# Kernel tuning notes

Measured on AMD Instinct MI355X. Metric: run time of the kernel, lower is better.

Reference implementation:

```python
import jax, jax.numpy as jnp
import numpy as np

N_NODES = 100000
N_EDGES = 1000000
IN_DIM = 64
OUT_DIM = 64
EDGE_DIM = 16
LN_EPS = 1e-5
GINE_EPS = 0.0  # PyG GINEConv default eps


def setup_inputs() -> dict:
    key = jax.random.key(0)
    ks = jax.random.split(key, 10)
    s = lambda d: 1.0 / np.sqrt(d)
    x = jax.random.normal(ks[0], (N_NODES, IN_DIM), dtype=jnp.float32)
    edge_index = jax.random.randint(ks[1], (2, N_EDGES), 0, N_NODES, dtype=jnp.int64)
    edge_attr = jax.random.normal(ks[2], (N_EDGES, EDGE_DIM), dtype=jnp.float32)
    # GINEConv internal edge projection Linear(edge_dim, in_dim)
    We = jax.random.uniform(ks[3], (EDGE_DIM, IN_DIM), jnp.float32, -s(EDGE_DIM), s(EDGE_DIM))
    be = jax.random.uniform(ks[4], (IN_DIM,), jnp.float32, -s(EDGE_DIM), s(EDGE_DIM))
    # MLP: Linear(in_dim, out_dim) -> ReLU -> Linear(out_dim, out_dim)
    W1 = jax.random.uniform(ks[5], (IN_DIM, OUT_DIM), jnp.float32, -s(IN_DIM), s(IN_DIM))
    b1 = jax.random.uniform(ks[6], (OUT_DIM,), jnp.float32, -s(IN_DIM), s(IN_DIM))
    W2 = jax.random.uniform(ks[7], (OUT_DIM, OUT_DIM), jnp.float32, -s(OUT_DIM), s(OUT_DIM))
    b2 = jax.random.uniform(ks[8], (OUT_DIM,), jnp.float32, -s(OUT_DIM), s(OUT_DIM))
    ln_gamma = jnp.ones((OUT_DIM,), jnp.float32)
    ln_beta = jnp.zeros((OUT_DIM,), jnp.float32)
    return {"x": x, "edge_index": edge_index, "edge_attr": edge_attr,
            "We": We, "be": be, "W1": W1, "b1": b1, "W2": W2, "b2": b2,
            "ln_gamma": ln_gamma, "ln_beta": ln_beta}


def reference(x, edge_index, edge_attr, We, be, W1, b1, W2, b2, ln_gamma, ln_beta):
    src, dst = edge_index[0], edge_index[1]
    # message: ReLU(x_j + lin(edge_attr))  [E, IN_DIM]
    msg = jax.nn.relu(x[src] + edge_attr @ We + be)
    # scatter-sum into target nodes  [N, IN_DIM]
    aggr = jax.ops.segment_sum(msg, dst, num_segments=x.shape[0])
    h = (1.0 + GINE_EPS) * x + aggr
    # MLP
    h = jax.nn.relu(h @ W1 + b1) @ W2 + b2
    # LayerNorm over last dim
    mu = jnp.mean(h, axis=-1, keepdims=True)
    var = jnp.var(h, axis=-1, keepdims=True)
    h = (h - mu) * jax.lax.rsqrt(var + LN_EPS) * ln_gamma + ln_beta
    return jax.nn.relu(h)
```

## Files before the change

### kernel.cpp

```cpp
#include <hip/hip_runtime.h>

typedef short short8 __attribute__((ext_vector_type(8)));
typedef float f32x4 __attribute__((ext_vector_type(4)));

__device__ __forceinline__ float bf2f(unsigned short b) {
    union { unsigned u; float f; } c;
    c.u = ((unsigned)b) << 16;
    return c.f;
}

__device__ __forceinline__ unsigned short f2bf(float x) {
    union { float f; unsigned u; } c;
    c.f = x;
    unsigned u = c.u;
    u += 0x7fffu + ((u >> 16) & 1u);
    return (unsigned short)(u >> 16);
}

__device__ __forceinline__ float loadf(const void* p, long long i, unsigned isbf) {
    if (isbf) return bf2f(((const unsigned short*)p)[i]);
    return ((const float*)p)[i];
}

__device__ __forceinline__ f32x4 mfma16(short8 a, short8 b, f32x4 c) {
    return __builtin_amdgcn_mfma_f32_16x16x32_bf16(a, b, c, 0, 0, 0);
}

__device__ __forceinline__ float dotbf(uint4 ea, uint4 eb, const float* Wcol) {
    unsigned wds[8] = {ea.x, ea.y, ea.z, ea.w, eb.x, eb.y, eb.z, eb.w};
    float acc = 0.f;
    #pragma unroll
    for (int q = 0; q < 8; ++q) {
        union { unsigned u; float f; } clo, chi;
        clo.u = wds[q] << 16;
        chi.u = wds[q] & 0xffff0000u;
        acc += clo.f * Wcol[2 * q] + chi.f * Wcol[2 * q + 1];
    }
    return acc;
}

__device__ __forceinline__ float dotf32(const float* eap, const float* Wcol) {
    f32x4 e0 = ((const f32x4*)eap)[0];
    f32x4 e1 = ((const f32x4*)eap)[1];
    f32x4 e2 = ((const f32x4*)eap)[2];
    f32x4 e3 = ((const f32x4*)eap)[3];
    float ea[16] = {e0[0], e0[1], e0[2], e0[3],
                    e1[0], e1[1], e1[2], e1[3],
                    e2[0], e2[1], e2[2], e2[3],
                    e3[0], e3[1], e3[2], e3[3]};
    float acc = 0.f;
    #pragma unroll
    for (int k = 0; k < 16; ++k) acc += ea[k] * Wcol[k];
    return acc;
}

__global__ void gine_flag_kernel(const unsigned* gm_bits, const unsigned* ei_bits,
                                 unsigned* flags) {
    if (blockIdx.x == 0 && threadIdx.x == 0) {
        flags[0] = (gm_bits[0] == 0x3F803F80u) ? 1u : 0u;
        unsigned o = 0;
        for (int k = 0; k < 8; ++k) o |= ei_bits[2 * k + 1];
        flags[1] = (o == 0u) ? 1u : 0u;
    }
}

__global__ void gine_zero_kernel(float* p, int n) {
    int t = blockIdx.x * blockDim.x + threadIdx.x;
    if (t < n) p[t] = 0.0f;
}

__global__ void gine_prep_kernel(const void* W1, const void* b1,
                                 const void* W2, const void* b2,
                                 const void* gm, const void* bt,
                                 const void* We, const void* be,
                                 const unsigned* flags,
                                 unsigned short* W1B, unsigned short* W2B,
                                 float* vecs) {
    int t = blockIdx.x * blockDim.x + threadIdx.x;
    unsigned isbf = flags[0];
    if (t < 8192) {
        int which = t >> 12;
        int u = t & 4095;
        int j = u & 7, L = (u >> 3) & 63, ktnt = u >> 9;
        int kt = ktnt >> 2, nt = ktnt & 3;
        int k = kt * 32 + (L >> 4) * 8 + j;
        int c = nt * 16 + (L & 15);
        const void* W = which ? W2 : W1;
        unsigned short v = f2bf(loadf(W, k * 64 + c, isbf));
        if (which) W2B[u] = v; else W1B[u] = v;
    } else if (t < 8448) {
        int u = t - 8192;
        const void* s = (u < 64) ? b1 : (u < 128) ? b2 : (u < 192) ? gm : bt;
        vecs[u] = loadf(s, u & 63, isbf);
    } else if (t < 8512) {
        vecs[256 + (t - 8448)] = loadf(be, t - 8448, isbf);
    } else if (t < 9536) {
        int u = t - 8512;
        vecs[320 + u] = loadf(We, u, isbf);
    }
}

__global__ void gine_hist_kernel(const void* edge_index, const unsigned* flags,
                                 int* count, int E, int N) {
    int t = blockIdx.x * blockDim.x + threadIdx.x;
    int stride = gridDim.x * blockDim.x;
    unsigned is64 = flags[1];
    for (int e = t; e < E; e += stride) {
        long long dst = is64 ? ((const long long*)edge_index)[E + e]
                             : (long long)((const int*)edge_index)[E + e];
        if (dst >= 0 && dst < N) atomicAdd(&count[(int)dst], 1);
    }
}

__global__ void gine_scan1_kernel(const int* count, int* row_start, int* bsum,
                                  int N) {
    __shared__ int s[256];
    int t = threadIdx.x;
    int i = blockIdx.x * 256 + t;
    int v = (i < N) ? count[i] : 0;
    s[t] = v;
    __syncthreads();
    for (int off = 1; off < 256; off <<= 1) {
        int u = (t >= off) ? s[t - off] : 0;
        __syncthreads();
        s[t] += u;
        __syncthreads();
    }
    if (i < N) row_start[i] = s[t] - v;
    if (t == 255) bsum[blockIdx.x] = s[255];
}

__global__ void gine_scan2_kernel(int* bsum, int* bscan, int* row_start,
                                  int nb, int N) {
    __shared__ int s[512];
    int t = threadIdx.x;
    int v = (t < nb) ? bsum[t] : 0;
    s[t] = v;
    __syncthreads();
    for (int off = 1; off < 512; off <<= 1) {
        int u = (t >= off) ? s[t - off] : 0;
        __syncthreads();
        s[t] += u;
        __syncthreads();
    }
    if (t < nb) bscan[t] = s[t] - v;
    if (t == nb - 1) row_start[N] = s[t];
}

__global__ void gine_scan3_kernel(int* row_start, int* cursor,
                                  const int* bscan, int N) {
    int i = blockIdx.x * 256 + threadIdx.x;
    if (i < N) {
        int r = row_start[i] + bscan[blockIdx.x];
        row_start[i] = r;
        cursor[i] = r;
    }
}

__global__ void gine_scatter_kernel(const void* edge_index, const unsigned* flags,
                                    int* cursor, unsigned long long* sorted,
                                    int E, int N) {
    int t = blockIdx.x * blockDim.x + threadIdx.x;
    int stride = gridDim.x * blockDim.x;
    unsigned is64 = flags[1];
    for (int e = t; e < E; e += stride) {
        long long src, dst;
        if (is64) {
            src = ((const long long*)edge_index)[e];
            dst = ((const long long*)edge_index)[E + e];
        } else {
            src = ((const int*)edge_index)[e];
            dst = ((const int*)edge_index)[E + e];
        }
        if (dst < 0 || dst >= N) continue;
        if (src < 0) src = 0;
        if (src >= N) src = N - 1;
        int pos = atomicAdd(&cursor[(int)dst], 1);
        sorted[pos] = ((unsigned long long)(unsigned)e << 32) | (unsigned long long)(unsigned)src;
    }
}

__global__ void gine_scatter2_kernel(const void* edge_index, const void* edge_attr,
                                     const unsigned* flags,
                                     int* cursor, unsigned long long* sorted,
                                     unsigned short* ea_perm, int E, int N) {
    int t = blockIdx.x * blockDim.x + threadIdx.x;
    int stride = gridDim.x * blockDim.x;
    unsigned is64 = flags[1];
    unsigned isbf = flags[0];
    for (int e = t; e < E; e += stride) {
        long long src, dst;
        if (is64) {
            src = ((const long long*)edge_index)[e];
            dst = ((const long long*)edge_index)[E + e];
        } else {
            src = ((const int*)edge_index)[e];
            dst = ((const int*)edge_index)[E + e];
        }
        if (dst < 0 || dst >= N) continue;
        if (src < 0) src = 0;
        if (src >= N) src = N - 1;
        int pos = atomicAdd(&cursor[(int)dst], 1);
        sorted[pos] = ((unsigned long long)(unsigned)e << 32) | (unsigned long long)(unsigned)src;
        if (isbf) {
            const uint4* er = (const uint4*)((const unsigned short*)edge_attr
                                             + (size_t)e * 16);
            uint4 r0 = er[0];
            uint4 r1 = er[1];
            uint4* wp = (uint4*)(ea_perm + (size_t)pos * 16);
            wp[0] = r0;
            wp[1] = r1;
        }
    }
}

__global__ __launch_bounds__(256) void gine_gather2_kernel(
        const void* x, const void* edge_attr,
        const unsigned long long* sorted, const unsigned short* ea_perm,
        const int* row_start, const float* vecs,
        const unsigned* flags, float* h, int N) {
    int w = threadIdx.x >> 6;
    int lane = threadIdx.x & 63;
    int gw = blockIdx.x * 4 + w;
    int nwaves = gridDim.x * 4;
    unsigned isbf = flags[0];

    float Wcol[16];
    #pragma unroll
    for (int k = 0; k < 16; ++k) Wcol[k] = vecs[320 + k * 64 + lane];
    float bev = vecs[256 + lane];

    if (isbf) {
        const unsigned short* xb = (const unsigned short*)x;
        for (int v = gw; v < N; v += nwaves) {
            int beg = row_start[v];
            int end = row_start[v + 1];
            float a0 = bf2f(xb[(size_t)v * 64 + lane]);
            float a1 = 0.f;
            int i = beg;
            for (; i + 2 <= end; i += 2) {
                unsigned long long c0 = sorted[i];
                unsigned long long c1 = sorted[i + 1];
                int src0 = (int)(c0 & 0xffffffffULL);
                int src1 = (int)(c1 & 0xffffffffULL);

                const uint4* p = (const uint4*)(ea_perm + (size_t)i * 16);
                uint4 e00 = p[0], e01 = p[1];
                uint4 e10 = p[2], e11 = p[3];

                float xv0 = bf2f(xb[(size_t)src0 * 64 + lane]);
                float xv1 = bf2f(xb[(size_t)src1 * 64 + lane]);

                float m0 = dotbf(e00, e01, Wcol);
                float m1 = dotbf(e10, e11, Wcol);
                m0 += bev + xv0; if (m0 < 0.f) m0 = 0.f; a0 += m0;
                m1 += bev + xv1; if (m1 < 0.f) m1 = 0.f; a1 += m1;
            }
            for (; i < end; ++i) {
                unsigned long long c = sorted[i];
                int src = (int)(c & 0xffffffffULL);
                const uint4* p = (const uint4*)(ea_perm + (size_t)i * 16);
                uint4 e0 = p[0], e1 = p[1];
                float xv = bf2f(xb[(size_t)src * 64 + lane]);
                float m = dotbf(e0, e1, Wcol);
                m += bev + xv;
                if (m < 0.f) m = 0.f;
                a0 += m;
            }
            h[(long long)v * 64 + lane] = a0 + a1;
        }
    } else {
        const float* xf  = (const float*)x;
        const float* eaf = (const float*)edge_attr;
        for (int v = gw; v < N; v += nwaves) {
            int beg = row_start[v];
            int end = row_start[v + 1];
            float a0 = xf[(size_t)v * 64 + lane];
            float a1 = 0.f;
            int i = beg;
            for (; i + 2 <= end; i += 2) {
                unsigned long long c0 = sorted[i];
                unsigned long long c1 = sorted[i + 1];
                int src0 = (int)(c0 & 0xffffffffULL), eid0 = (int)(c0 >> 32);
                int src1 = (int)(c1 & 0xffffffffULL), eid1 = (int)(c1 >> 32);
                float xv0 = xf[(size_t)src0 * 64 + lane];
                float xv1 = xf[(size_t)src1 * 64 + lane];
                float m0 = dotf32(eaf + (size_t)eid0 * 16, Wcol);
                float m1 = dotf32(eaf + (size_t)eid1 * 16, Wcol);
                m0 += bev + xv0; if (m0 < 0.f) m0 = 0.f; a0 += m0;
                m1 += bev + xv1; if (m1 < 0.f) m1 = 0.f; a1 += m1;
            }
            for (; i < end; ++i) {
                unsigned long long c = sorted[i];
                int src = (int)(c & 0xffffffffULL);
                int eid = (int)(c >> 32);
                float xv = xf[(size_t)src * 64 + lane];
                float m = dotf32(eaf + (size_t)eid * 16, Wcol);
                m += bev + xv;
                if (m < 0.f) m = 0.f;
                a0 += m;
            }
            h[(long long)v * 64 + lane] = a0 + a1;
        }
    }
}

__global__ __launch_bounds__(256, 4) void gine_gather_kernel(
        const void* x, const void* edge_attr,
        const unsigned long long* sorted,
        const int* row_start, const float* vecs,
        const unsigned* flags, float* h, int N) {
    int w = threadIdx.x >> 6;
    int lane = threadIdx.x & 63;
    int gw = blockIdx.x * 4 + w;
    int nwaves = gridDim.x * 4;
    unsigned isbf = flags[0];

    float Wcol[16];
    #pragma unroll
    for (int k = 0; k < 16; ++k) Wcol[k] = vecs[320 + k * 64 + lane];
    float bev = vecs[256 + lane];

    if (isbf) {
        const unsigned short* xb  = (const unsigned short*)x;
        const unsigned short* eab = (const unsigned short*)edge_attr;
        for (int v = gw; v < N; v += nwaves) {
            int beg = row_start[v];
            int end = row_start[v + 1];
            float a0 = bf2f(xb[(size_t)v * 64 + lane]);
            float a1 = 0.f, a2 = 0.f, a3 = 0.f;
            int i = beg;
            for (; i + 4 <= end; i += 4) {
                unsigned long long c0 = sorted[i];
                unsigned long long c1 = sorted[i + 1];
                unsigned long long c2 = sorted[i + 2];
                unsigned long long c3 = sorted[i + 3];
                int src0 = (int)(c0 & 0xffffffffULL), eid0 = (int)(c0 >> 32);
                int src1 = (int)(c1 & 0xffffffffULL), eid1 = (int)(c1 >> 32);
                int src2 = (int)(c2 & 0xffffffffULL), eid2 = (int)(c2 >> 32);
                int src3 = (int)(c3 & 0xffffffffULL), eid3 = (int)(c3 >> 32);

                float xv0 = bf2f(xb[(size_t)src0 * 64 + lane]);
                float xv1 = bf2f(xb[(size_t)src1 * 64 + lane]);
                float xv2 = bf2f(xb[(size_t)src2 * 64 + lane]);
                float xv3 = bf2f(xb[(size_t)src3 * 64 + lane]);

                const uint4* p0 = (const uint4*)(eab + (size_t)eid0 * 16);
                const uint4* p1 = (const uint4*)(eab + (size_t)eid1 * 16);
                const uint4* p2 = (const uint4*)(eab + (size_t)eid2 * 16);
                const uint4* p3 = (const uint4*)(eab + (size_t)eid3 * 16);
                uint4 e00 = p0[0], e01 = p0[1];
                uint4 e10 = p1[0], e11 = p1[1];
                uint4 e20 = p2[0], e21 = p2[1];
                uint4 e30 = p3[0], e31 = p3[1];

                float m0 = dotbf(e00, e01, Wcol);
                float m1 = dotbf(e10, e11, Wcol);
                float m2 = dotbf(e20, e21, Wcol);
                float m3 = dotbf(e30, e31, Wcol);
                m0 += bev + xv0; if (m0 < 0.f) m0 = 0.f; a0 += m0;
                m1 += bev + xv1; if (m1 < 0.f) m1 = 0.f; a1 += m1;
                m2 += bev + xv2; if (m2 < 0.f) m2 = 0.f; a2 += m2;
                m3 += bev + xv3; if (m3 < 0.f) m3 = 0.f; a3 += m3;
            }
            for (; i < end; ++i) {
                unsigned long long c = sorted[i];
                int src = (int)(c & 0xffffffffULL);
                int eid = (int)(c >> 32);
                float xv = bf2f(xb[(size_t)src * 64 + lane]);
                const uint4* p0 = (const uint4*)(eab + (size_t)eid * 16);
                uint4 e0 = p0[0], e1 = p0[1];
                float m = dotbf(e0, e1, Wcol);
                m += bev + xv;
                if (m < 0.f) m = 0.f;
                a0 += m;
            }
            h[(long long)v * 64 + lane] = (a0 + a1) + (a2 + a3);
        }
    } else {
        const float* xf  = (const float*)x;
        const float* eaf = (const float*)edge_attr;
        for (int v = gw; v < N; v += nwaves) {
            int beg = row_start[v];
            int end = row_start[v + 1];
            float a0 = xf[(size_t)v * 64 + lane];
            float a1 = 0.f;
            int i = beg;
            for (; i + 2 <= end; i += 2) {
                unsigned long long c0 = sorted[i];
                unsigned long long c1 = sorted[i + 1];
                int src0 = (int)(c0 & 0xffffffffULL), eid0 = (int)(c0 >> 32);
                int src1 = (int)(c1 & 0xffffffffULL), eid1 = (int)(c1 >> 32);
                float xv0 = xf[(size_t)src0 * 64 + lane];
                float xv1 = xf[(size_t)src1 * 64 + lane];
                float m0 = dotf32(eaf + (size_t)eid0 * 16, Wcol);
                float m1 = dotf32(eaf + (size_t)eid1 * 16, Wcol);
                m0 += bev + xv0; if (m0 < 0.f) m0 = 0.f; a0 += m0;
                m1 += bev + xv1; if (m1 < 0.f) m1 = 0.f; a1 += m1;
            }
            for (; i < end; ++i) {
                unsigned long long c = sorted[i];
                int src = (int)(c & 0xffffffffULL);
                int eid = (int)(c >> 32);
                float xv = xf[(size_t)src * 64 + lane];
                float m = dotf32(eaf + (size_t)eid * 16, Wcol);
                m += bev + xv;
                if (m < 0.f) m = 0.f;
                a0 += m;
            }
            h[(long long)v * 64 + lane] = a0 + a1;
        }
    }
}

__global__ void GINEBlock_49795850830259_kernel(
    const void* x, const void* edge_index, const void* edge_attr,
    const void* We, const void* be, const unsigned* flags,
    float* aggr, int E, int N, int n0, int n1) {
    int wid  = (blockIdx.x * blockDim.x + threadIdx.x) >> 6;
    int lane = threadIdx.x & 63;
    if (wid >= E) return;

    unsigned isbf = flags[0];
    unsigned is64 = flags[1];

    long long src, dst;
    if (is64) {
        src = ((const long long*)edge_index)[wid];
        dst = ((const long long*)edge_index)[E + wid];
    } else {
        src = ((const int*)edge_index)[wid];
        dst = ((const int*)edge_index)[E + wid];
    }
    if (src < 0 || src >= N || dst < n0 || dst >= n1) return;

    float eav = 0.0f;
    if (lane < 16) eav = loadf(edge_attr, (long long)wid * 16 + lane, isbf);

    float acc = loadf(be, lane, isbf);
    for (int k = 0; k < 16; ++k)
        acc += __shfl(eav, k, 64) * loadf(We, k * 64 + lane, isbf);

    acc += loadf(x, src * 64 + lane, isbf);
    if (acc < 0.0f) acc = 0.0f;

    atomicAdd(aggr + (dst - n0) * 64 + lane, acc);
}

__global__ void gine_addx_kernel(const void* x, float* aggr,
                                 const unsigned* flags, int n0, int n1) {
    int t = blockIdx.x * blockDim.x + threadIdx.x;
    int total = (n1 - n0) * 64;
    if (t >= total) return;
    unsigned isbf = flags[0];
    aggr[t] += loadf(x, (long long)n0 * 64 + t, isbf);
}

__global__ __launch_bounds__(256) void gine_node_mfma_kernel(
    const float* h, const unsigned short* W1B, const unsigned short* W2B,
    const float* vecs, const unsigned* flags, void* out, int n0, int n1) {
    __shared__ float Tlds[4][16 * 68];
    int w = threadIdx.x >> 6;
    int L = threadIdx.x & 63;
    int g = L >> 4, m = L & 15;
    int nb = n0 + (blockIdx.x * 4 + w) * 16;
    if (nb >= n1) return;
    unsigned isbf = flags[0];

    const float* b1f = vecs;
    const float* b2f = vecs + 64;
    const float* gmf = vecs + 128;
    const float* btf = vecs + 192;

    int node = nb + m;
    if (node >= n1) node = n1 - 1;
    long long rel = node - n0;

    short8 ahi[2], alo[2];
    for (int kt = 0; kt < 2; ++kt) {
        int fb = kt * 32 + g * 8;
        const float* hp = h + rel * 64 + fb;
        f32x4 a0 = *(const f32x4*)hp;
        f32x4 a1 = *(const f32x4*)(hp + 4);
        for (int j = 0; j < 8; ++j) {
            float hv = (j < 4) ? a0[j] : a1[j - 4];
            unsigned short hb = f2bf(hv);
            float lo = hv - bf2f(hb);
            ahi[kt][j] = (short)hb;
            alo[kt][j] = (short)f2bf(lo);
        }
    }

    float t16[16];
    for (int nt = 0; nt < 4; ++nt) {
        short8 bp0 = *(const short8*)(W1B + ((size_t)(0 * 4 + nt) * 64 + L) * 8);
        short8 bp1 = *(const short8*)(W1B + ((size_t)(1 * 4 + nt) * 64 + L) * 8);
        f32x4 acc = {0.f, 0.f, 0.f, 0.f};
        acc = mfma16(ahi[0], bp0, acc);
        acc = mfma16(ahi[1], bp1, acc);
        acc = mfma16(alo[0], bp0, acc);
        acc = mfma16(alo[1], bp1, acc);
        float bias = b1f[nt * 16 + m];
        for (int r = 0; r < 4; ++r) {
            float v = acc[r] + bias;
            t16[nt * 4 + r] = v > 0.f ? v : 0.f;
        }
    }

    float* tl = Tlds[w];
    for (int nt = 0; nt < 4; ++nt)
        for (int r = 0; r < 4; ++r)
            tl[(g * 4 + r) * 68 + nt * 16 + m] = t16[nt * 4 + r];

    short8 thi[2], tlo[2];
    for (int kt = 0; kt < 2; ++kt) {
        const float* rp = tl + m * 68 + kt * 32 + g * 8;
        f32x4 v0 = *(const f32x4*)rp;
        f32x4 v1 = *(const f32x4*)(rp + 4);
        for (int j = 0; j < 8; ++j) {
            float hv = (j < 4) ? v0[j] : v1[j - 4];
            unsigned short hb = f2bf(hv);
            float lo = hv - bf2f(hb);
            thi[kt][j] = (short)hb;
            tlo[kt][j] = (short)f2bf(lo);
        }
    }

    float o16[16];
    for (int nt = 0; nt < 4; ++nt) {
        short8 bp0 = *(const short8*)(W2B + ((size_t)(0 * 4 + nt) * 64 + L) * 8);
        short8 bp1 = *(const short8*)(W2B + ((size_t)(1 * 4 + nt) * 64 + L) * 8);
        f32x4 acc = {0.f, 0.f, 0.f, 0.f};
        acc = mfma16(thi[0], bp0, acc);
        acc = mfma16(thi[1], bp1, acc);
        acc = mfma16(tlo[0], bp0, acc);
        acc = mfma16(tlo[1], bp1, acc);
        float bias = b2f[nt * 16 + m];
        for (int r = 0; r < 4; ++r) o16[nt * 4 + r] = acc[r] + bias;
    }

    for (int r = 0; r < 4; ++r) {
        float s = o16[r] + o16[4 + r] + o16[8 + r] + o16[12 + r];
        s += __shfl_xor(s, 1, 64);
        s += __shfl_xor(s, 2, 64);
        s += __shfl_xor(s, 4, 64);
        s += __shfl_xor(s, 8, 64);
        float mu = s * (1.0f / 64.0f);
        float v = 0.f;
        for (int nt = 0; nt < 4; ++nt) {
            float d = o16[nt * 4 + r] - mu;
            v += d * d;
        }
        v += __shfl_xor(v, 1, 64);
        v += __shfl_xor(v, 2, 64);
        v += __shfl_xor(v, 4, 64);
        v += __shfl_xor(v, 8, 64);
        float inv = rsqrtf(v * (1.0f / 64.0f) + 1e-5f);
        int nodeR = nb + g * 4 + r;
        if (nodeR < n1) {
            for (int nt = 0; nt < 4; ++nt) {
                int c = nt * 16 + m;
                float rr = (o16[nt * 4 + r] - mu) * inv * gmf[c] + btf[c];
                if (rr < 0.f) rr = 0.f;
                long long oidx = (long long)nodeR * 64 + c;
                if (isbf) ((unsigned short*)out)[oidx] = f2bf(rr);
                else      ((float*)out)[oidx] = rr;
            }
        }
    }
}

static inline size_t align256(size_t a) { return (a + 255) & ~(size_t)255; }

extern "C" void kernel_launch(void* const* d_in, const int* in_sizes, int n_in,
                              void* d_out, int out_size, void* d_ws, size_t ws_size,
                              hipStream_t stream) {
    const void* x          = d_in[0];
    const void* edge_index = d_in[1];
    const void* edge_attr  = d_in[2];
    const void* We         = d_in[3];
    const void* be         = d_in[4];
    const void* W1         = d_in[5];
    const void* b1         = d_in[6];
    const void* W2         = d_in[7];
    const void* b2         = d_in[8];
    const void* gm         = d_in[9];
    const void* bt         = d_in[10];

    const int N = in_sizes[0] / 64;
    const int E = in_sizes[1] / 2;

    unsigned* flags     = (unsigned*)d_ws;
    unsigned short* W1B = (unsigned short*)((char*)d_ws + 256);
    unsigned short* W2B = W1B + 4096;
    float* vecs         = (float*)(W2B + 4096);
    int* bsum           = (int*)((char*)d_ws + 24576);
    int* bscan          = bsum + 1024;

    gine_flag_kernel<<<1, 64, 0, stream>>>((const unsigned*)gm,
                                           (const unsigned*)edge_index, flags);
    gine_prep_kernel<<<38, 256, 0, stream>>>(W1, b1, W2, b2, gm, bt, We, be,
                                             flags, W1B, W2B, vecs);

    int nb = (N + 255) / 256;
    int node_blocks = (N + 63) / 64;
    int gblocks = (N + 15) / 16;
    if (gblocks > 6250) gblocks = 6250;

    size_t o_count  = 32768;
    size_t o_row    = o_count + align256((size_t)N * 4);
    size_t o_cursor = o_row + align256((size_t)(N + 1) * 4);
    size_t o_sorted = o_cursor + align256((size_t)N * 4);
    size_t o_eap    = o_sorted + align256((size_t)E * 8);
    size_t o_h1     = o_eap;
    size_t o_h2     = o_eap + align256((size_t)E * 32);
    size_t need1    = o_h1 + (size_t)N * 256;
    size_t need2    = o_h2 + (size_t)N * 256;

    if (ws_size >= need1 && nb <= 512) {
        int* count    = (int*)((char*)d_ws + o_count);
        int* row_start= (int*)((char*)d_ws + o_row);
        int* cursor   = (int*)((char*)d_ws + o_cursor);
        unsigned long long* sorted = (unsigned long long*)((char*)d_ws + o_sorted);
        bool tier2 = (ws_size >= need2);
        unsigned short* ea_perm = (unsigned short*)((char*)d_ws + o_eap);
        float* h = (float*)((char*)d_ws + (tier2 ? o_h2 : o_h1));

        gine_zero_kernel<<<(N + 255) / 256, 256, 0, stream>>>((float*)count, N);
        gine_hist_kernel<<<1024, 256, 0, stream>>>(edge_index, flags, count, E, N);
        gine_scan1_kernel<<<nb, 256, 0, stream>>>(count, row_start, bsum, N);
        gine_scan2_kernel<<<1, 512, 0, stream>>>(bsum, bscan, row_start, nb, N);
        gine_scan3_kernel<<<nb, 256, 0, stream>>>(row_start, cursor, bscan, N);
        if (tier2) {
            gine_scatter2_kernel<<<1024, 256, 0, stream>>>(edge_index, edge_attr,
                                                           flags, cursor, sorted,
                                                           ea_perm, E, N);
            gine_gather2_kernel<<<gblocks, 256, 0, stream>>>(x, edge_attr, sorted,
                                                             ea_perm, row_start,
                                                             vecs, flags, h, N);
        } else {
            gine_scatter_kernel<<<1024, 256, 0, stream>>>(edge_index, flags, cursor,
                                                          sorted, E, N);
            gine_gather_kernel<<<gblocks, 256, 0, stream>>>(x, edge_attr, sorted,
                                                            row_start, vecs, flags,
                                                            h, N);
        }
        gine_node_mfma_kernel<<<node_blocks, 256, 0, stream>>>(
            h, W1B, W2B, vecs, flags, d_out, 0, N);
        return;
    }

    float* aggr = (float*)((char*)d_ws + 32768);
    long long usable = (ws_size > 32768) ? (long long)(ws_size - 32768) : 0;
    long long ncll = (usable / 256) & ~63LL;
    int NC = (ncll > N) ? N : (int)ncll;
    if (NC < 64) return;

    long long edge_threads = (long long)E * 64;
    int edge_blocks = (int)((edge_threads + 255) / 256);

    for (int n0 = 0; n0 < N; n0 += NC) {
        int n1 = n0 + NC; if (n1 > N) n1 = N;
        int chunk = n1 - n0;
        int n_aggr = chunk * 64;

        gine_zero_kernel<<<(n_aggr + 255) / 256, 256, 0, stream>>>(aggr, n_aggr);
        GINEBlock_49795850830259_kernel<<<edge_blocks, 256, 0, stream>>>(
            x, edge_index, edge_attr, We, be, flags, aggr, E, N, n0, n1);
        gine_addx_kernel<<<(n_aggr + 255) / 256, 256, 0, stream>>>(
            x, aggr, flags, n0, n1);
        int chunk_blocks = (chunk + 63) / 64;
        gine_node_mfma_kernel<<<chunk_blocks, 256, 0, stream>>>(
            aggr, W1B, W2B, vecs, flags, d_out, n0, n1);
    }
}
```

Baseline: 460.6 us.

## Tile edge gather by source-node range in multiple passes for cache locality

Edges are bucketed by (destination, source tile) using a per-node per-tile histogram, scan and scatter. The gather then runs one pass per source tile (up to 8 tiles), so each pass only touches a slice of x that can stay in cache. Partial sums are accumulated in h across passes. This adds NT extra kernel launches, repeated row metadata reads and a larger tile-count array, in exchange for better reuse of gathered x rows.

Result: slower. 724.3 us (+57.3%).

```diff
diff --git a/kernel.cpp b/kernel.cpp
--- a/kernel.cpp
+++ b/kernel.cpp
@@ -100,6 +100,212 @@
     }
 }
 
+__global__ void gine_histT_kernel(const void* edge_index, const unsigned* flags,
+                                  int* tileCnt, int E, int N, int NT, int sh) {
+    int t = blockIdx.x * blockDim.x + threadIdx.x;
+    int stride = gridDim.x * blockDim.x;
+    unsigned is64 = flags[1];
+    for (int e = t; e < E; e += stride) {
+        long long src, dst;
+        if (is64) {
+            src = ((const long long*)edge_index)[e];
+            dst = ((const long long*)edge_index)[E + e];
+        } else {
+            src = ((const int*)edge_index)[e];
+            dst = ((const int*)edge_index)[E + e];
+        }
+        if (dst < 0 || dst >= N) continue;
+        if (src < 0) src = 0;
+        if (src >= N) src = N - 1;
+        int tl = (int)(src >> sh);
+        atomicAdd(&tileCnt[(size_t)dst * NT + tl], 1);
+    }
+}
+
+__global__ void gine_scan1T_kernel(const int* tileCnt, int* row_start, int* bsum,
+                                   int N, int NT) {
+    __shared__ int s[256];
+    int t = threadIdx.x;
+    int i = blockIdx.x * 256 + t;
+    int v = 0;
+    if (i < N) {
+        for (int q = 0; q < NT; ++q) v += tileCnt[(size_t)i * NT + q];
+    }
+    s[t] = v;
+    __syncthreads();
+    for (int off = 1; off < 256; off <<= 1) {
+        int u = (t >= off) ? s[t - off] : 0;
+        __syncthreads();
+        s[t] += u;
+        __syncthreads();
+    }
+    if (i < N) row_start[i] = s[t] - v;
+    if (t == 255) bsum[blockIdx.x] = s[255];
+}
+
+__global__ void gine_scan2_kernel(int* bsum, int* bscan, int* row_start,
+                                  int nb, int N) {
+    __shared__ int s[512];
+    int t = threadIdx.x;
+    int v = (t < nb) ? bsum[t] : 0;
+    s[t] = v;
+    __syncthreads();
+    for (int off = 1; off < 512; off <<= 1) {
+        int u = (t >= off) ? s[t - off] : 0;
+        __syncthreads();
+        s[t] += u;
+        __syncthreads();
+    }
+    if (t < nb) bscan[t] = s[t] - v;
+    if (t == nb - 1) row_start[N] = s[t];
+}
+
+__global__ void gine_scan3b_kernel(int* row_start, const int* bscan, int N) {
+    int i = blockIdx.x * 256 + threadIdx.x;
+    if (i < N) row_start[i] += bscan[blockIdx.x];
+}
+
+__global__ void gine_scan3_kernel(int* row_start, int* cursor,
+                                  const int* bscan, int N) {
+    int i = blockIdx.x * 256 + threadIdx.x;
+    if (i < N) {
+        int r = row_start[i] + bscan[blockIdx.x];
+        row_start[i] = r;
+        cursor[i] = r;
+    }
+}
+
+__global__ void gine_tstart_kernel(const int* row_start, int* tileCnt,
+                                   int* tstart, int N, int NT) {
+    int v = blockIdx.x * blockDim.x + threadIdx.x;
+    if (v >= N) return;
+    int base = row_start[v];
+    for (int t = 0; t < NT; ++t) {
+        int c = tileCnt[(size_t)v * NT + t];
+        tstart[(size_t)v * NT + t] = base;
+        tileCnt[(size_t)v * NT + t] = base;
+        base += c;
+    }
+}
+
+__global__ void gine_scatterT_kernel(const void* edge_index, const void* edge_attr,
+                                     const unsigned* flags, int* cursor,
+                                     unsigned long long* meta,
+                                     unsigned short* ea_perm,
+                                     int E, int N, int NT, int sh) {
+    int t = blockIdx.x * blockDim.x + threadIdx.x;
+    int stride = gridDim.x * blockDim.x;
+    unsigned is64 = flags[1];
+    unsigned isbf = flags[0];
+    for (int e = t; e < E; e += stride) {
+        long long src, dst;
+        if (is64) {
+            src = ((const long long*)edge_index)[e];
+            dst = ((const long long*)edge_index)[E + e];
+        } else {
+            src = ((const int*)edge_index)[e];
+            dst = ((const int*)edge_index)[E + e];
+        }
+        if (dst < 0 || dst >= N) continue;
+        if (src < 0) src = 0;
+        if (src >= N) src = N - 1;
+        int tl = (int)(src >> sh);
+        int pos = atomicAdd(&cursor[(size_t)dst * NT + tl], 1);
+        meta[pos] = ((unsigned long long)(unsigned)e << 32)
+                  | (unsigned long long)(unsigned)src;
+        if (isbf) {
+            const uint4* er = (const uint4*)((const unsigned short*)edge_attr
+                                             + (size_t)e * 16);
+            uint4 r0 = er[0];
+            uint4 r1 = er[1];
+            uint4* wp = (uint4*)(ea_perm + (size_t)pos * 16);
+            wp[0] = r0;
+            wp[1] = r1;
+        }
+    }
+}
+
+__global__ __launch_bounds__(256, 4) void gine_gpass_kernel(
+        const void* x, const void* edge_attr,
+        const unsigned long long* meta, const unsigned short* ea_perm,
+        const int* tstart, const int* row_start,
+        const float* vecs, const unsigned* flags,
+        float* h, int N, int NT, int t) {
+    int w = threadIdx.x >> 6;
+    int lane = threadIdx.x & 63;
+    int gw = blockIdx.x * 4 + w;
+    int nwaves = gridDim.x * 4;
+    unsigned isbf = flags[0];
+
+    float Wcol[16];
+    #pragma unroll
+    for (int k = 0; k < 16; ++k) Wcol[k] = vecs[320 + k * 64 + lane];
+    float bev = vecs[256 + lane];
+
+    if (isbf) {
+        const unsigned short* xb = (const unsigned short*)x;
+        for (int v = gw; v < N; v += nwaves) {
+            int beg = tstart[(size_t)v * NT + t];
+            int end = (t == NT - 1) ? row_start[v + 1]
+                                    : tstart[(size_t)v * NT + t + 1];
+            if (t > 0 && beg == end) continue;
+            float a0 = (t == 0) ? bf2f(xb[(size_t)v * 64 + lane])
+                                : h[(size_t)v * 64 + lane];
+            float a1 = 0.f;
+            int i = beg;
+            for (; i + 2 <= end; i += 2) {
+                unsigned long long c0 = meta[i];
+                unsigned long long c1 = meta[i + 1];
+                int src0 = (int)(c0 & 0xffffffffULL);
+                int src1 = (int)(c1 & 0xffffffffULL);
+                const uint4* p = (const uint4*)(ea_perm + (size_t)i * 16);
+                uint4 e00 = p[0], e01 = p[1];
+                uint4 e10 = p[2], e11 = p[3];
+                float xv0 = bf2f(xb[(size_t)src0 * 64 + lane]);
+                float xv1 = bf2f(xb[(size_t)src1 * 64 + lane]);
+                float m0 = dotbf(e00, e01, Wcol) + bev + xv0;
+                float m1 = dotbf(e10, e11, Wcol) + bev + xv1;
+                if (m0 < 0.f) m0 = 0.f;
+                if (m1 < 0.f) m1 = 0.f;
+                a0 += m0;
+                a1 += m1;
+            }
+            if (i < end) {
+                unsigned long long c = meta[i];
+                int src = (int)(c & 0xffffffffULL);
+                const uint4* p = (const uint4*)(ea_perm + (size_t)i * 16);
+                uint4 e0 = p[0], e1 = p[1];
+                float xv = bf2f(xb[(size_t)src * 64 + lane]);
+                float m = dotbf(e0, e1, Wcol) + bev + xv;
+                if (m < 0.f) m = 0.f;
+                a0 += m;
+            }
+            h[(size_t)v * 64 + lane] = a0 + a1;
+        }
+    } else {
+        const float* xf  = (const float*)x;
+        const float* eaf = (const float*)edge_attr;
+        for (int v = gw; v < N; v += nwaves) {
+            int beg = tstart[(size_t)v * NT + t];
+            int end = (t == NT - 1) ? row_start[v + 1]
+                                    : tstart[(size_t)v * NT + t + 1];
+            if (t > 0 && beg == end) continue;
+            float a0 = (t == 0) ? xf[(size_t)v * 64 + lane]
+                                : h[(size_t)v * 64 + lane];
+            for (int i = beg; i < end; ++i) {
+                unsigned long long c = meta[i];
+                int src = (int)(c & 0xffffffffULL);
+                int eid = (int)(c >> 32);
+                float xv = xf[(size_t)src * 64 + lane];
+                float m = dotf32(eaf + (size_t)eid * 16, Wcol) + bev + xv;
+                if (m < 0.f) m = 0.f;
+                a0 += m;
+            }
+            h[(size_t)v * 64 + lane] = a0;
+        }
+    }
+}
+
 __global__ void gine_hist_kernel(const void* edge_index, const unsigned* flags,
                                  int* count, int E, int N) {
     int t = blockIdx.x * blockDim.x + threadIdx.x;
@@ -128,33 +334,6 @@
     }
     if (i < N) row_start[i] = s[t] - v;
     if (t == 255) bsum[blockIdx.x] = s[255];
-}
-
-__global__ void gine_scan2_kernel(int* bsum, int* bscan, int* row_start,
-                                  int nb, int N) {
-    __shared__ int s[512];
-    int t = threadIdx.x;
-    int v = (t < nb) ? bsum[t] : 0;
-    s[t] = v;
-    __syncthreads();
-    for (int off = 1; off < 512; off <<= 1) {
-        int u = (t >= off) ? s[t - off] : 0;
-        __syncthreads();
-        s[t] += u;
-        __syncthreads();
-    }
-    if (t < nb) bscan[t] = s[t] - v;
-    if (t == nb - 1) row_start[N] = s[t];
-}
-
-__global__ void gine_scan3_kernel(int* row_start, int* cursor,
-                                  const int* bscan, int N) {
-    int i = blockIdx.x * 256 + threadIdx.x;
-    if (i < N) {
-        int r = row_start[i] + bscan[blockIdx.x];
-        row_start[i] = r;
-        cursor[i] = r;
-    }
 }
 
 __global__ void gine_scatter_kernel(const void* edge_index, const unsigned* flags,
@@ -180,43 +359,9 @@
     }
 }
 
-__global__ void gine_scatter2_kernel(const void* edge_index, const void* edge_attr,
-                                     const unsigned* flags,
-                                     int* cursor, unsigned long long* sorted,
-                                     unsigned short* ea_perm, int E, int N) {
-    int t = blockIdx.x * blockDim.x + threadIdx.x;
-    int stride = gridDim.x * blockDim.x;
-    unsigned is64 = flags[1];
-    unsigned isbf = flags[0];
-    for (int e = t; e < E; e += stride) {
-        long long src, dst;
-        if (is64) {
-            src = ((const long long*)edge_index)[e];
-            dst = ((const long long*)edge_index)[E + e];
-        } else {
-            src = ((const int*)edge_index)[e];
-            dst = ((const int*)edge_index)[E + e];
-        }
-        if (dst < 0 || dst >= N) continue;
-        if (src < 0) src = 0;
-        if (src >= N) src = N - 1;
-        int pos = atomicAdd(&cursor[(int)dst], 1);
-        sorted[pos] = ((unsigned long long)(unsigned)e << 32) | (unsigned long long)(unsigned)src;
-        if (isbf) {
-            const uint4* er = (const uint4*)((const unsigned short*)edge_attr
-                                             + (size_t)e * 16);
-            uint4 r0 = er[0];
-            uint4 r1 = er[1];
-            uint4* wp = (uint4*)(ea_perm + (size_t)pos * 16);
-            wp[0] = r0;
-            wp[1] = r1;
-        }
-    }
-}
-
-__global__ __launch_bounds__(256) void gine_gather2_kernel(
+__global__ __launch_bounds__(256, 4) void gine_gather_kernel(
         const void* x, const void* edge_attr,
-        const unsigned long long* sorted, const unsigned short* ea_perm,
+        const unsigned long long* sorted,
         const int* row_start, const float* vecs,
         const unsigned* flags, float* h, int N) {
     int w = threadIdx.x >> 6;
@@ -231,43 +376,60 @@
     float bev = vecs[256 + lane];
 
     if (isbf) {
-        const unsigned short* xb = (const unsigned short*)x;
+        const unsigned short* xb  = (const unsigned short*)x;
+        const unsigned short* eab = (const unsigned short*)edge_attr;
         for (int v = gw; v < N; v += nwaves) {
             int beg = row_start[v];
             int end = row_start[v + 1];
             float a0 = bf2f(xb[(size_t)v * 64 + lane]);
-            float a1 = 0.f;
+            float a1 = 0.f, a2 = 0.f, a3 = 0.f;
             int i = beg;
-            for (; i + 2 <= end; i += 2) {
+            for (; i + 4 <= end; i += 4) {
                 unsigned long long c0 = sorted[i];
                 unsigned long long c1 = sorted[i + 1];
-                int src0 = (int)(c0 & 0xffffffffULL);
-                int src1 = (int)(c1 & 0xffffffffULL);
-
-                const uint4* p = (const uint4*)(ea_perm + (size_t)i * 16);
-                uint4 e00 = p[0], e01 = p[1];
-                uint4 e10 = p[2], e11 = p[3];
+                unsigned long long c2 = sorted[i + 2];
+                unsigned long long c3 = sorted[i + 3];
+                int src0 = (int)(c0 & 0xffffffffULL), eid0 = (int)(c0 >> 32);
+                int src1 = (int)(c1 & 0xffffffffULL), eid1 = (int)(c1 >> 32);
+                int src2 = (int)(c2 & 0xffffffffULL), eid2 = (int)(c2 >> 32);
+                int src3 = (int)(c3 & 0xffffffffULL), eid3 = (int)(c3 >> 32);
 
                 float xv0 = bf2f(xb[(size_t)src0 * 64 + lane]);
                 float xv1 = bf2f(xb[(size_t)src1 * 64 + lane]);
+                float xv2 = bf2f(xb[(size_t)src2 * 64 + lane]);
+                float xv3 = bf2f(xb[(size_t)src3 * 64 + lane]);
+
+                const uint4* p0 = (const uint4*)(eab + (size_t)eid0 * 16);
+                const uint4* p1 = (const uint4*)(eab + (size_t)eid1 * 16);
+                const uint4* p2 = (const uint4*)(eab + (size_t)eid2 * 16);
+                const uint4* p3 = (const uint4*)(eab + (size_t)eid3 * 16);
+                uint4 e00 = p0[0], e01 = p0[1];
+                uint4 e10 = p1[0], e11 = p1[1];
+                uint4 e20 = p2[0], e21 = p2[1];
+                uint4 e30 = p3[0], e31 = p3[1];
 
                 float m0 = dotbf(e00, e01, Wcol);
                 float m1 = dotbf(e10, e11, Wcol);
+                float m2 = dotbf(e20, e21, Wcol);
+                float m3 = dotbf(e30, e31, Wcol);
                 m0 += bev + xv0; if (m0 < 0.f) m0 = 0.f; a0 += m0;
                 m1 += bev + xv1; if (m1 < 0.f) m1 = 0.f; a1 += m1;
+                m2 += bev + xv2; if (m2 < 0.f) m2 = 0.f; a2 += m2;
+                m3 += bev + xv3; if (m3 < 0.f) m3 = 0.f; a3 += m3;
             }
             for (; i < end; ++i) {
                 unsigned long long c = sorted[i];
                 int src = (int)(c & 0xffffffffULL);
-                const uint4* p = (const uint4*)(ea_perm + (size_t)i * 16);
-                uint4 e0 = p[0], e1 = p[1];
+                int eid = (int)(c >> 32);
                 float xv = bf2f(xb[(size_t)src * 64 + lane]);
+                const uint4* p0 = (const uint4*)(eab + (size_t)eid * 16);
+                uint4 e0 = p0[0], e1 = p0[1];
                 float m = dotbf(e0, e1, Wcol);
                 m += bev + xv;
                 if (m < 0.f) m = 0.f;
                 a0 += m;
             }
-            h[(long long)v * 64 + lane] = a0 + a1;
+            h[(long long)v * 64 + lane] = (a0 + a1) + (a2 + a3);
         }
     } else {
         const float* xf  = (const float*)x;
@@ -305,114 +467,6 @@
     }
 }
 
-__global__ __launch_bounds__(256, 4) void gine_gather_kernel(
-        const void* x, const void* edge_attr,
-        const unsigned long long* sorted,
-        const int* row_start, const float* vecs,
-        const unsigned* flags, float* h, int N) {
-    int w = threadIdx.x >> 6;
-    int lane = threadIdx.x & 63;
-    int gw = blockIdx.x * 4 + w;
-    int nwaves = gridDim.x * 4;
-    unsigned isbf = flags[0];
-
-    float Wcol[16];
-    #pragma unroll
-    for (int k = 0; k < 16; ++k) Wcol[k] = vecs[320 + k * 64 + lane];
-    float bev = vecs[256 + lane];
-
-    if (isbf) {
-        const unsigned short* xb  = (const unsigned short*)x;
-        const unsigned short* eab = (const unsigned short*)edge_attr;
-        for (int v = gw; v < N; v += nwaves) {
-            int beg = row_start[v];
-            int end = row_start[v + 1];
-            float a0 = bf2f(xb[(size_t)v * 64 + lane]);
-            float a1 = 0.f, a2 = 0.f, a3 = 0.f;
-            int i = beg;
-            for (; i + 4 <= end; i += 4) {
-                unsigned long long c0 = sorted[i];
-                unsigned long long c1 = sorted[i + 1];
-                unsigned long long c2 = sorted[i + 2];
-                unsigned long long c3 = sorted[i + 3];
-                int src0 = (int)(c0 & 0xffffffffULL), eid0 = (int)(c0 >> 32);
-                int src1 = (int)(c1 & 0xffffffffULL), eid1 = (int)(c1 >> 32);
-                int src2 = (int)(c2 & 0xffffffffULL), eid2 = (int)(c2 >> 32);
-                int src3 = (int)(c3 & 0xffffffffULL), eid3 = (int)(c3 >> 32);
-
-                float xv0 = bf2f(xb[(size_t)src0 * 64 + lane]);
-                float xv1 = bf2f(xb[(size_t)src1 * 64 + lane]);
-                float xv2 = bf2f(xb[(size_t)src2 * 64 + lane]);
-                float xv3 = bf2f(xb[(size_t)src3 * 64 + lane]);
-
-                const uint4* p0 = (const uint4*)(eab + (size_t)eid0 * 16);
-                const uint4* p1 = (const uint4*)(eab + (size_t)eid1 * 16);
-                const uint4* p2 = (const uint4*)(eab + (size_t)eid2 * 16);
-                const uint4* p3 = (const uint4*)(eab + (size_t)eid3 * 16);
-                uint4 e00 = p0[0], e01 = p0[1];
-                uint4 e10 = p1[0], e11 = p1[1];
-                uint4 e20 = p2[0], e21 = p2[1];
-                uint4 e30 = p3[0], e31 = p3[1];
-
-                float m0 = dotbf(e00, e01, Wcol);
-                float m1 = dotbf(e10, e11, Wcol);
-                float m2 = dotbf(e20, e21, Wcol);
-                float m3 = dotbf(e30, e31, Wcol);
-                m0 += bev + xv0; if (m0 < 0.f) m0 = 0.f; a0 += m0;
-                m1 += bev + xv1; if (m1 < 0.f) m1 = 0.f; a1 += m1;
-                m2 += bev + xv2; if (m2 < 0.f) m2 = 0.f; a2 += m2;
-                m3 += bev + xv3; if (m3 < 0.f) m3 = 0.f; a3 += m3;
-            }
-            for (; i < end; ++i) {
-                unsigned long long c = sorted[i];
-                int src = (int)(c & 0xffffffffULL);
-                int eid = (int)(c >> 32);
-                float xv = bf2f(xb[(size_t)src * 64 + lane]);
-                const uint4* p0 = (const uint4*)(eab + (size_t)eid * 16);
-                uint4 e0 = p0[0], e1 = p0[1];
-                float m = dotbf(e0, e1, Wcol);
-                m += bev + xv;
-                if (m < 0.f) m = 0.f;
-                a0 += m;
-            }
-            h[(long long)v * 64 + lane] = (a0 + a1) + (a2 + a3);
-        }
-    } else {
-        const float* xf  = (const float*)x;
-        const float* eaf = (const float*)edge_attr;
-        for (int v = gw; v < N; v += nwaves) {
-            int beg = row_start[v];
-            int end = row_start[v + 1];
-            float a0 = xf[(size_t)v * 64 + lane];
-            float a1 = 0.f;
-            int i = beg;
-            for (; i + 2 <= end; i += 2) {
-                unsigned long long c0 = sorted[i];
-                unsigned long long c1 = sorted[i + 1];
-                int src0 = (int)(c0 & 0xffffffffULL), eid0 = (int)(c0 >> 32);
-                int src1 = (int)(c1 & 0xffffffffULL), eid1 = (int)(c1 >> 32);
-                float xv0 = xf[(size_t)src0 * 64 + lane];
-                float xv1 = xf[(size_t)src1 * 64 + lane];
-                float m0 = dotf32(eaf + (size_t)eid0 * 16, Wcol);
-                float m1 = dotf32(eaf + (size_t)eid1 * 16, Wcol);
-                m0 += bev + xv0; if (m0 < 0.f) m0 = 0.f; a0 += m0;
-                m1 += bev + xv1; if (m1 < 0.f) m1 = 0.f; a1 += m1;
-            }
-            for (; i < end; ++i) {
-                unsigned long long c = sorted[i];
-                int src = (int)(c & 0xffffffffULL);
-                int eid = (int)(c >> 32);
-                float xv = xf[(size_t)src * 64 + lane];
-                float m = dotf32(eaf + (size_t)eid * 16, Wcol);
-                m += bev + xv;
-                if (m < 0.f) m = 0.f;
-                a0 += m;
-            }
-            h[(long long)v * 64 + lane] = a0 + a1;
-        }
-    }
-}
-
 __global__ void GINEBlock_49795850830259_kernel(
     const void* x, const void* edge_index, const void* edge_attr,
     const void* We, const void* be, const unsigned* flags,
@@ -590,6 +644,10 @@
     const int N = in_sizes[0] / 64;
     const int E = in_sizes[1] / 2;
 
+    int sh = 14;
+    while ((((long long)(N - 1) >> sh) + 1) > 8) sh++;
+    const int NT = (int)(((long long)(N - 1) >> sh) + 1);
+
     unsigned* flags     = (unsigned*)d_ws;
     unsigned short* W1B = (unsigned short*)((char*)d_ws + 256);
     unsigned short* W2B = W1B + 4096;
@@ -607,44 +665,69 @@
     int gblocks = (N + 15) / 16;
     if (gblocks > 6250) gblocks = 6250;
 
+    size_t a_tc   = 32768;
+    size_t a_row  = a_tc + align256((size_t)N * NT * 4);
+    size_t a_ts   = a_row + align256((size_t)(N + 1) * 4);
+    size_t a_meta = a_ts + align256((size_t)N * NT * 4);
+    size_t a_eap  = a_meta + align256((size_t)E * 8);
+    size_t a_h    = a_eap + align256((size_t)E * 32);
+    size_t needA  = a_h + (size_t)N * 256;
+
+    if (ws_size >= needA && nb <= 512) {
+        int* tileCnt  = (int*)((char*)d_ws + a_tc);
+        int* row_start= (int*)((char*)d_ws + a_row);
+        int* tstart   = (int*)((char*)d_ws + a_ts);
+        unsigned long long* meta = (unsigned long long*)((char*)d_ws + a_meta);
+        unsigned short* ea_perm  = (unsigned short*)((char*)d_ws + a_eap);
+        float* h      = (float*)((char*)d_ws + a_h);
+
+        gine_zero_kernel<<<((size_t)N * NT + 255) / 256, 256, 0, stream>>>(
+            (float*)tileCnt, N * NT);
+        gine_histT_kernel<<<1024, 256, 0, stream>>>(edge_index, flags, tileCnt,
+                                                    E, N, NT, sh);
+        gine_scan1T_kernel<<<nb, 256, 0, stream>>>(tileCnt, row_start, bsum,
+                                                   N, NT);
+        gine_scan2_kernel<<<1, 512, 0, stream>>>(bsum, bscan, row_start, nb, N);
+        gine_scan3b_kernel<<<nb, 256, 0, stream>>>(row_start, bscan, N);
+        gine_tstart_kernel<<<(N + 255) / 256, 256, 0, stream>>>(
+            row_start, tileCnt, tstart, N, NT);
+        gine_scatterT_kernel<<<1024, 256, 0, stream>>>(edge_index, edge_attr,
+                                                       flags, tileCnt, meta,
+                                                       ea_perm, E, N, NT, sh);
+        for (int t = 0; t < NT; ++t) {
+            gine_gpass_kernel<<<gblocks, 256, 0, stream>>>(
+                x, edge_attr, meta, ea_perm, tstart, row_start,
+                vecs, flags, h, N, NT, t);
+        }
+        gine_node_mfma_kernel<<<node_blocks, 256, 0, stream>>>(
+            h, W1B, W2B, vecs, flags, d_out, 0, N);
+        return;
+    }
+
     size_t o_count  = 32768;
     size_t o_row    = o_count + align256((size_t)N * 4);
     size_t o_cursor = o_row + align256((size_t)(N + 1) * 4);
     size_t o_sorted = o_cursor + align256((size_t)N * 4);
-    size_t o_eap    = o_sorted + align256((size_t)E * 8);
-    size_t o_h1     = o_eap;
-    size_t o_h2     = o_eap + align256((size_t)E * 32);
-    size_t need1    = o_h1 + (size_t)N * 256;
-    size_t need2    = o_h2 + (size_t)N * 256;
-
-    if (ws_size >= need1 && nb <= 512) {
+    size_t o_h      = o_sorted + align256((size_t)E * 8);
+    size_t needB    = o_h + (size_t)N * 256;
+
+    if (ws_size >= needB && nb <= 512) {
         int* count    = (int*)((char*)d_ws + o_count);
         int* row_start= (int*)((char*)d_ws + o_row);
         int* cursor   = (int*)((char*)d_ws + o_cursor);
         unsigned long long* sorted = (unsigned long long*)((char*)d_ws + o_sorted);
-        bool tier2 = (ws_size >= need2);
-        unsigned short* ea_perm = (unsigned short*)((char*)d_ws + o_eap);
-        float* h = (float*)((char*)d_ws + (tier2 ? o_h2 : o_h1));
+        float* h      = (float*)((char*)d_ws + o_h);
 
         gine_zero_kernel<<<(N + 255) / 256, 256, 0, stream>>>((float*)count, N);
         gine_hist_kernel<<<1024, 256, 0, stream>>>(edge_index, flags, count, E, N);
         gine_scan1_kernel<<<nb, 256, 0, stream>>>(count, row_start, bsum, N);
         gine_scan2_kernel<<<1, 512, 0, stream>>>(bsum, bscan, row_start, nb, N);
         gine_scan3_kernel<<<nb, 256, 0, stream>>>(row_start, cursor, bscan, N);
-        if (tier2) {
-            gine_scatter2_kernel<<<1024, 256, 0, stream>>>(edge_index, edge_attr,
-                                                           flags, cursor, sorted,
-                                                           ea_perm, E, N);
-            gine_gather2_kernel<<<gblocks, 256, 0, stream>>>(x, edge_attr, sorted,
-                                                             ea_perm, row_start,
-                                                             vecs, flags, h, N);
-        } else {
-            gine_scatter_kernel<<<1024, 256, 0, stream>>>(edge_index, flags, cursor,
-                                                          sorted, E, N);
-            gine_gather_kernel<<<gblocks, 256, 0, stream>>>(x, edge_attr, sorted,
-                                                            row_start, vecs, flags,
-                                                            h, N);
-        }
+        gine_scatter_kernel<<<1024, 256, 0, stream>>>(edge_index, flags, cursor,
+                                                      sorted, E, N);
+        gine_gather_kernel<<<gblocks, 256, 0, stream>>>(x, edge_attr, sorted,
+                                                        row_start, vecs, flags,
+                                                        h, N);
         gine_node_mfma_kernel<<<node_blocks, 256, 0, stream>>>(
             h, W1B, W2B, vecs, flags, d_out, 0, N);
         return;
```
